# Optimization experiments

Measured on AMD Instinct MI355X. Metric: run time of the kernel, lower is better.

The kernel has to match this reference:

```python
import jax, jax.numpy as jnp
import numpy as np

D_MODEL = 1024
NUM_HEADS = 16
HEAD_DIM = D_MODEL // NUM_HEADS


def setup_inputs() -> dict:
    key = jax.random.key(0)
    kx, kq, kk, kv, ko = jax.random.split(key, 5)
    B, T = 2, 2048
    scale = 1.0 / np.sqrt(D_MODEL)
    return {
        "x": jax.random.normal(kx, (B, T, D_MODEL), dtype=jnp.float32),
        "wq": jax.random.normal(kq, (D_MODEL, D_MODEL), dtype=jnp.float32) * scale,
        "wk": jax.random.normal(kk, (D_MODEL, D_MODEL), dtype=jnp.float32) * scale,
        "wv": jax.random.normal(kv, (D_MODEL, D_MODEL), dtype=jnp.float32) * scale,
        "wo": jax.random.normal(ko, (D_MODEL, D_MODEL), dtype=jnp.float32) * scale,
    }


def _split_heads(x):
    b, t, _ = x.shape
    return x.reshape(b, t, NUM_HEADS, HEAD_DIM).transpose(0, 2, 1, 3)  # [b,h,t,d]


def reference(x, wq, wk, wv, wo):
    q = _split_heads(x @ wq)
    k = _split_heads(x @ wk)
    v = _split_heads(x @ wv)
    inv_sqrt_d = jnp.asarray(1.0 / np.sqrt(HEAD_DIM), x.dtype)
    scores = jnp.einsum("bhqd,bhkd->bhqk", q, k) * inv_sqrt_d
    weights = jax.nn.softmax(scores, axis=-1)  # dropout rate 0.0 -> identity
    out = jnp.einsum("bhqk,bhkd->bhqd", weights, v)
    b, h, t, d = out.shape
    out = out.transpose(0, 2, 1, 3).reshape(b, t, D_MODEL)
    return out @ wo
```

## Files before the change

kernel.cpp:

```cpp
#include <hip/hip_runtime.h>
#include <stdint.h>

using bf16   = __bf16;
using bf16x8 = __bf16 __attribute__((ext_vector_type(8)));
using bf16x4 = __bf16 __attribute__((ext_vector_type(4)));
using f32x4  = float  __attribute__((ext_vector_type(4)));
using f32x16 = float  __attribute__((ext_vector_type(16)));
using u32x4  = uint32_t __attribute__((ext_vector_type(4)));

#define DM 1024
#define T_ 2048
#define NH 16

__device__ __forceinline__ void gl_lds16(const void* g, void* l) {
  __builtin_amdgcn_global_load_lds(
      (__attribute__((address_space(1))) void*)g,
      (__attribute__((address_space(3))) void*)l, 16, 0, 0);
}

__device__ __forceinline__ f32x4 mfma16(bf16x8 a, bf16x8 b, f32x4 c) {
  return __builtin_amdgcn_mfma_f32_16x16x32_bf16(a, b, c, 0, 0, 0);
}
__device__ __forceinline__ f32x16 mfma32(bf16x8 a, bf16x8 b, f32x16 c) {
  return __builtin_amdgcn_mfma_f32_32x32x16_bf16(a, b, c, 0, 0, 0);
}
__device__ __forceinline__ uint32_t cvtpk(float lo, float hi) {
  uint32_t r;
  asm volatile("v_cvt_pk_bf16_f32 %0, %1, %2" : "=v"(r) : "v"(lo), "v"(hi));
  return r;
}

__global__ __launch_bounds__(256)
void k_cast_x(const float* __restrict__ x, bf16* __restrict__ xb) {
  const size_t i = (size_t)blockIdx.x * 256 + threadIdx.x;
  const float4 a = *(const float4*)(x + i * 8);
  const float4 c = *(const float4*)(x + i * 8 + 4);
  bf16x8 v;
  v[0] = (bf16)a.x; v[1] = (bf16)a.y; v[2] = (bf16)a.z; v[3] = (bf16)a.w;
  v[4] = (bf16)c.x; v[5] = (bf16)c.y; v[6] = (bf16)c.z; v[7] = (bf16)c.w;
  *(bf16x8*)(xb + i * 8) = v;
}

__global__ __launch_bounds__(256)
void k_transpose_w4(const float* __restrict__ w0, const float* __restrict__ w1,
                    const float* __restrict__ w2, const float* __restrict__ w3,
                    bf16* __restrict__ wtq, bf16* __restrict__ wto) {
  const int z = blockIdx.z;
  const float* w = (z == 0) ? w0 : (z == 1) ? w1 : (z == 2) ? w2 : w3;
  bf16* wt = (z < 3) ? (wtq + (size_t)z * 1024 * 1024) : wto;
  const float scale = (z == 0) ? 0.125f * 1.44269504f : 1.0f;
  __shared__ float tile[64][68];
  const int tx = threadIdx.x & 15;
  const int ty = threadIdx.x >> 4;
  const int k0 = blockIdx.y * 64, n0 = blockIdx.x * 64;
#pragma unroll
  for (int j = 0; j < 4; ++j) {
    const int r = ty + 16 * j;
    const float4 v = *(const float4*)(w + (size_t)(k0 + r) * DM + n0 + tx * 4);
    tile[r][tx * 4 + 0] = v.x; tile[r][tx * 4 + 1] = v.y;
    tile[r][tx * 4 + 2] = v.z; tile[r][tx * 4 + 3] = v.w;
  }
  __syncthreads();
#pragma unroll
  for (int j = 0; j < 4; ++j) {
    const int r = ty + 16 * j;
    bf16x4 o;
    o[0] = (bf16)(tile[tx * 4 + 0][r] * scale);
    o[1] = (bf16)(tile[tx * 4 + 1][r] * scale);
    o[2] = (bf16)(tile[tx * 4 + 2][r] * scale);
    o[3] = (bf16)(tile[tx * 4 + 3][r] * scale);
    *(bf16x4*)(wt + (size_t)(n0 + r) * DM + k0 + tx * 4) = o;
  }
}

template<int MODE>
__global__ __launch_bounds__(256)
void k_gemm(const bf16* __restrict__ A, const bf16* __restrict__ BT,
            bf16* __restrict__ Qg, bf16* __restrict__ Kg, bf16* __restrict__ Vt,
            float* __restrict__ Cout) {
  constexpr int BN = (MODE == 0) ? 128 : 64;
  constexpr int NTW = BN / 32;
  __shared__ __align__(16) bf16 Ash[128 * 32];
  __shared__ __align__(16) bf16 Bsh[BN * 32];
  const int tn = blockIdx.x, tm = blockIdx.y;
  const int lane = threadIdx.x & 63, w = threadIdx.x >> 6;
  const int wm = w >> 1, wn = w & 1;
  const int r16 = lane & 15, g = lane >> 4;
  f32x4 acc[4][NTW] = {};
  const bf16* Arow = A + (size_t)tm * 128 * DM;
  const bf16* Brow = BT + (size_t)tn * BN * DM;
  for (int k0 = 0; k0 < DM; k0 += 32) {
#pragma unroll
    for (int t = 0; t < 2; ++t) {
      const int q = t * 256 + w * 64 + lane;
      gl_lds16(Arow + (size_t)(q >> 2) * DM + k0 + (q & 3) * 8, Ash + (t * 256 + w * 64) * 8);
    }
#pragma unroll
    for (int t = 0; t < BN / 64; ++t) {
      const int q = t * 256 + w * 64 + lane;
      gl_lds16(Brow + (size_t)(q >> 2) * DM + k0 + (q & 3) * 8, Bsh + (t * 256 + w * 64) * 8);
    }
    __syncthreads();
    bf16x8 af[4], bfr[NTW];
#pragma unroll
    for (int mt = 0; mt < 4; ++mt)
      af[mt] = *(const bf16x8*)(Ash + (wm * 64 + mt * 16 + r16) * 32 + g * 8);
#pragma unroll
    for (int nt = 0; nt < NTW; ++nt)
      bfr[nt] = *(const bf16x8*)(Bsh + (wn * (BN / 2) + nt * 16 + r16) * 32 + g * 8);
#pragma unroll
    for (int mt = 0; mt < 4; ++mt)
#pragma unroll
      for (int nt = 0; nt < NTW; ++nt)
        acc[mt][nt] = mfma16(af[mt], bfr[nt], acc[mt][nt]);
    __syncthreads();
  }
#pragma unroll
  for (int mt = 0; mt < 4; ++mt) {
#pragma unroll
    for (int nt = 0; nt < NTW; ++nt) {
      const int ncol = tn * BN + wn * (BN / 2) + nt * 16 + r16;
      const int m0 = tm * 128 + wm * 64 + mt * 16 + g * 4;
      if (MODE == 0) {
        const int which = ncol >> 10, nl = ncol & 1023;
        const int h = nl >> 6, d = nl & 63;
        const int b = m0 >> 11, t0 = m0 & 2047;
        if (which == 2) {
          bf16x4 pv;
#pragma unroll
          for (int r = 0; r < 4; ++r) pv[r] = (bf16)acc[mt][nt][r];
          *(bf16x4*)(Vt + ((size_t)(b * NH + h) * 64 + d) * T_ + t0) = pv;
        } else {
          bf16* dst = (which == 0) ? Qg : Kg;
#pragma unroll
          for (int r = 0; r < 4; ++r)
            dst[(((size_t)(b * NH + h) * T_ + t0 + r) << 6) + d] = (bf16)acc[mt][nt][r];
        }
      } else {
#pragma unroll
        for (int r = 0; r < 4; ++r)
          Cout[(size_t)(m0 + r) * DM + ncol] = acc[mt][nt][r];
      }
    }
  }
}

__global__ __launch_bounds__(512)
void k_attn(const bf16* __restrict__ Qg, const bf16* __restrict__ Kg,
            const bf16* __restrict__ Vtr, bf16* __restrict__ Ao) {
  __shared__ __align__(16) bf16 Ksh[2][2][64 * 64];
  __shared__ __align__(16) bf16 Vsh[2][2][64 * 64];
  __shared__ float Lsh[4][64];
  const int qt = blockIdx.x, bh = blockIdx.y;
  const int lane = threadIdx.x & 63, w = threadIdx.x >> 6;
  const int qw = w & 3, kh = w >> 2;
  const int l31 = lane & 31, hi = lane >> 5;
  const bf16* Qb = Qg + (size_t)bh * T_ * 64;
  const bf16* Kb = Kg + (size_t)bh * T_ * 64;
  const bf16* Vb = Vtr + (size_t)bh * 64 * T_;
  const int q0 = qt * 128 + qw * 32;
  bf16x8 qb[4];
#pragma unroll
  for (int s = 0; s < 4; ++s)
    qb[s] = *(const bf16x8*)(Qb + (size_t)(q0 + l31) * 64 + s * 16 + hi * 8);
  f32x16 o0 = {}, o1 = {};
  float llocal = 0.f;
  const int swz31 = (l31 & 7) << 4;
  const int srow = lane >> 3;
  const int schunk = (lane & 7) ^ srow;

  auto stage = [&](int buf, int ti) {
#pragma unroll
    for (int j = 0; j < 2; ++j) {
      const int idx = qw * 2 + j;
      const int row = idx * 8 + srow;
      gl_lds16(Kb + (size_t)(ti * 64 + row) * 64 + schunk * 8, &Ksh[kh][buf][idx * 512]);
      gl_lds16(Vb + (size_t)row * T_ + ti * 64 + schunk * 8, &Vsh[kh][buf][idx * 512]);
    }
  };

  constexpr int NTH = T_ / 64 / 2;
  stage(0, kh * NTH);
  __syncthreads();
  for (int i = 0; i < NTH; ++i) {
    const int cur = i & 1;
    if (i + 1 < NTH) stage(cur ^ 1, kh * NTH + i + 1);
    const char* Kc = (const char*)Ksh[kh][cur];
    const char* Vc = (const char*)Vsh[kh][cur];
    f32x16 st0 = {}, st1 = {};
    __builtin_amdgcn_s_setprio(1);
#pragma unroll
    for (int s = 0; s < 4; ++s) {
      const int cb = (s * 32 + hi * 16) ^ swz31;
      const bf16x8 k0 = *(const bf16x8*)(Kc + l31 * 128 + cb);
      const bf16x8 k1 = *(const bf16x8*)(Kc + (32 + l31) * 128 + cb);
      st0 = mfma32(k0, qb[s], st0);
      st1 = mfma32(k1, qb[s], st1);
    }
    __builtin_amdgcn_s_setprio(0);
#pragma unroll
    for (int r = 0; r < 16; ++r) {
      st0[r] = __builtin_amdgcn_exp2f(st0[r]); llocal += st0[r];
    }
#pragma unroll
    for (int r = 0; r < 16; ++r) {
      st1[r] = __builtin_amdgcn_exp2f(st1[r]); llocal += st1[r];
    }
    __builtin_amdgcn_s_setprio(1);
#pragma unroll
    for (int s = 0; s < 4; ++s) {
      const f32x16& sv = (s < 2) ? st0 : st1;
      const int si = (s & 1) * 8;
      uint32_t a0 = cvtpk(sv[si + 0], sv[si + 1]);
      uint32_t a1 = cvtpk(sv[si + 2], sv[si + 3]);
      uint32_t b0 = cvtpk(sv[si + 4], sv[si + 5]);
      uint32_t b1 = cvtpk(sv[si + 6], sv[si + 7]);
      asm volatile("v_permlane32_swap_b32 %0, %1" : "+v"(a0), "+v"(b0));
      asm volatile("v_permlane32_swap_b32 %0, %1" : "+v"(a1), "+v"(b1));
      u32x4 fr; fr[0] = a0; fr[1] = a1; fr[2] = b0; fr[3] = b1;
      const bf16x8 pas = __builtin_bit_cast(bf16x8, fr);
      const int cb = (s * 32 + hi * 16) ^ swz31;
      const bf16x8 v0 = *(const bf16x8*)(Vc + l31 * 128 + cb);
      const bf16x8 v1 = *(const bf16x8*)(Vc + (32 + l31) * 128 + cb);
      o0 = mfma32(pas, v0, o0);
      o1 = mfma32(pas, v1, o1);
    }
    __builtin_amdgcn_s_setprio(0);
    __syncthreads();
  }
  float* cb = (float*)&Ksh[0][0][0] + qw * 2048;
  if (kh == 1) {
#pragma unroll
    for (int r = 0; r < 16; ++r) {
      cb[r * 64 + lane]        = o0[r];
      cb[(16 + r) * 64 + lane] = o1[r];
    }
    Lsh[qw][lane] = llocal;
  }
  __syncthreads();
  if (kh == 0) {
    llocal += Lsh[qw][lane];
#pragma unroll
    for (int r = 0; r < 16; ++r) {
      o0[r] += cb[r * 64 + lane];
      o1[r] += cb[(16 + r) * 64 + lane];
    }
    llocal += __shfl_xor(llocal, 32);
    const int b = bh >> 4, h = bh & 15;
#pragma unroll
    for (int r = 0; r < 16; ++r) {
      const int qoff = (r & 3) + 8 * (r >> 2) + 4 * hi;
      const float linv = 1.f / __shfl(llocal, qoff);
      const size_t base = ((size_t)(b * T_ + q0 + qoff)) * DM + h * 64 + l31;
      Ao[base]      = (bf16)(o0[r] * linv);
      Ao[base + 32] = (bf16)(o1[r] * linv);
    }
  }
}

extern "C" void kernel_launch(void* const* d_in, const int* in_sizes, int n_in,
                              void* d_out, int out_size, void* d_ws, size_t ws_size,
                              hipStream_t stream) {
  const float* x  = (const float*)d_in[0];
  const float* wq = (const float*)d_in[1];
  const float* wk = (const float*)d_in[2];
  const float* wv = (const float*)d_in[3];
  const float* wo = (const float*)d_in[4];
  char* ws = (char*)d_ws;
  const size_t MB = 1024 * 1024;
  bf16* xb   = (bf16*)(ws + 0);
  bf16* wtq  = (bf16*)(ws + 8 * MB);
  bf16* wto  = (bf16*)(ws + 14 * MB);
  bf16* Qg   = (bf16*)(ws + 16 * MB);
  bf16* Kg   = (bf16*)(ws + 24 * MB);
  bf16* Vtr  = (bf16*)(ws + 32 * MB);

  k_cast_x<<<dim3(2048), dim3(256), 0, stream>>>(x, xb);
  k_transpose_w4<<<dim3(16, 16, 4), dim3(256), 0, stream>>>(wq, wk, wv, wo, wtq, wto);
  k_gemm<0><<<dim3(24, 32), dim3(256), 0, stream>>>(xb, wtq, Qg, Kg, Vtr, (float*)nullptr);
  k_attn<<<dim3(16, 32), dim3(512), 0, stream>>>(Qg, Kg, Vtr, xb);
  k_gemm<1><<<dim3(16, 32), dim3(256), 0, stream>>>(xb, wto, (bf16*)nullptr, (bf16*)nullptr,
                                                    (bf16*)nullptr, (float*)d_out);
}
```

Baseline: 122.3 us.

## Store K and V in MFMA fragment order so attention reads them linearly

The projection GEMM epilogue now writes K and V directly in the per-lane fragment order that the attention MFMAs consume, in 64-key tiles of 4096 elements. The attention kernel stages each tile with contiguous 16-byte loads and reads fragments with lane-linear LDS accesses. This removes the XOR swizzle and its address arithmetic, and is meant to avoid LDS bank conflicts. The cost is scattered, less coalesced stores in the GEMM epilogue, especially the 2-byte strided writes for K.

Result: no change. 122.6 us (+0.2%).

```diff
diff --git a/kernel.cpp b/kernel.cpp
--- a/kernel.cpp
+++ b/kernel.cpp
@@ -76,7 +76,7 @@
 template<int MODE>
 __global__ __launch_bounds__(256)
 void k_gemm(const bf16* __restrict__ A, const bf16* __restrict__ BT,
-            bf16* __restrict__ Qg, bf16* __restrict__ Kg, bf16* __restrict__ Vt,
+            bf16* __restrict__ Qg, bf16* __restrict__ Kf, bf16* __restrict__ Vf,
             float* __restrict__ Cout) {
   constexpr int BN = (MODE == 0) ? 128 : 64;
   constexpr int NTW = BN / 32;
@@ -125,16 +125,25 @@
         const int which = ncol >> 10, nl = ncol & 1023;
         const int h = nl >> 6, d = nl & 63;
         const int b = m0 >> 11, t0 = m0 & 2047;
+        const size_t hb = (size_t)(b * NH + h) * (T_ * 64);
         if (which == 2) {
+          const int kt = t0 >> 6, s = (t0 & 63) >> 4, hi2 = (t0 >> 3) & 1, j0 = t0 & 7;
+          const int dh = d >> 5, d31 = d & 31;
           bf16x4 pv;
 #pragma unroll
           for (int r = 0; r < 4; ++r) pv[r] = (bf16)acc[mt][nt][r];
-          *(bf16x4*)(Vt + ((size_t)(b * NH + h) * 64 + d) * T_ + t0) = pv;
+          *(bf16x4*)(Vf + hb + kt * 4096 + (s * 2 + dh) * 512 + (hi2 * 32 + d31) * 8 + j0) = pv;
+        } else if (which == 1) {
+          const int kt = t0 >> 6, kh2 = (t0 >> 5) & 1;
+          const int s = d >> 4, hi2 = (d >> 3) & 1, j = d & 7;
+          bf16* base = Kf + hb + kt * 4096 + (s * 2 + kh2) * 512 + hi2 * 256 + j;
+#pragma unroll
+          for (int r = 0; r < 4; ++r)
+            base[((t0 & 31) + r) * 8] = (bf16)acc[mt][nt][r];
         } else {
-          bf16* dst = (which == 0) ? Qg : Kg;
 #pragma unroll
           for (int r = 0; r < 4; ++r)
-            dst[(((size_t)(b * NH + h) * T_ + t0 + r) << 6) + d] = (bf16)acc[mt][nt][r];
+            Qg[hb + (size_t)(t0 + r) * 64 + d] = (bf16)acc[mt][nt][r];
         }
       } else {
 #pragma unroll
@@ -146,8 +155,8 @@
 }
 
 __global__ __launch_bounds__(512)
-void k_attn(const bf16* __restrict__ Qg, const bf16* __restrict__ Kg,
-            const bf16* __restrict__ Vtr, bf16* __restrict__ Ao) {
+void k_attn(const bf16* __restrict__ Qg, const bf16* __restrict__ Kf,
+            const bf16* __restrict__ Vf, bf16* __restrict__ Ao) {
   __shared__ __align__(16) bf16 Ksh[2][2][64 * 64];
   __shared__ __align__(16) bf16 Vsh[2][2][64 * 64];
   __shared__ float Lsh[4][64];
@@ -155,9 +164,9 @@
   const int lane = threadIdx.x & 63, w = threadIdx.x >> 6;
   const int qw = w & 3, kh = w >> 2;
   const int l31 = lane & 31, hi = lane >> 5;
-  const bf16* Qb = Qg + (size_t)bh * T_ * 64;
-  const bf16* Kb = Kg + (size_t)bh * T_ * 64;
-  const bf16* Vb = Vtr + (size_t)bh * 64 * T_;
+  const bf16* Qb  = Qg + (size_t)bh * T_ * 64;
+  const bf16* Kfh = Kf + (size_t)bh * T_ * 64;
+  const bf16* Vfh = Vf + (size_t)bh * T_ * 64;
   const int q0 = qt * 128 + qw * 32;
   bf16x8 qb[4];
 #pragma unroll
@@ -165,17 +174,13 @@
     qb[s] = *(const bf16x8*)(Qb + (size_t)(q0 + l31) * 64 + s * 16 + hi * 8);
   f32x16 o0 = {}, o1 = {};
   float llocal = 0.f;
-  const int swz31 = (l31 & 7) << 4;
-  const int srow = lane >> 3;
-  const int schunk = (lane & 7) ^ srow;
 
   auto stage = [&](int buf, int ti) {
 #pragma unroll
     for (int j = 0; j < 2; ++j) {
       const int idx = qw * 2 + j;
-      const int row = idx * 8 + srow;
-      gl_lds16(Kb + (size_t)(ti * 64 + row) * 64 + schunk * 8, &Ksh[kh][buf][idx * 512]);
-      gl_lds16(Vb + (size_t)row * T_ + ti * 64 + schunk * 8, &Vsh[kh][buf][idx * 512]);
+      gl_lds16(Kfh + (size_t)ti * 4096 + idx * 512 + lane * 8, &Ksh[kh][buf][idx * 512]);
+      gl_lds16(Vfh + (size_t)ti * 4096 + idx * 512 + lane * 8, &Vsh[kh][buf][idx * 512]);
     }
   };
 
@@ -185,15 +190,14 @@
   for (int i = 0; i < NTH; ++i) {
     const int cur = i & 1;
     if (i + 1 < NTH) stage(cur ^ 1, kh * NTH + i + 1);
-    const char* Kc = (const char*)Ksh[kh][cur];
-    const char* Vc = (const char*)Vsh[kh][cur];
+    const bf16* Kc = &Ksh[kh][cur][0];
+    const bf16* Vc = &Vsh[kh][cur][0];
     f32x16 st0 = {}, st1 = {};
     __builtin_amdgcn_s_setprio(1);
 #pragma unroll
     for (int s = 0; s < 4; ++s) {
-      const int cb = (s * 32 + hi * 16) ^ swz31;
-      const bf16x8 k0 = *(const bf16x8*)(Kc + l31 * 128 + cb);
-      const bf16x8 k1 = *(const bf16x8*)(Kc + (32 + l31) * 128 + cb);
+      const bf16x8 k0 = *(const bf16x8*)(Kc + (s * 2 + 0) * 512 + lane * 8);
+      const bf16x8 k1 = *(const bf16x8*)(Kc + (s * 2 + 1) * 512 + lane * 8);
       st0 = mfma32(k0, qb[s], st0);
       st1 = mfma32(k1, qb[s], st1);
     }
@@ -219,9 +223,8 @@
       asm volatile("v_permlane32_swap_b32 %0, %1" : "+v"(a1), "+v"(b1));
       u32x4 fr; fr[0] = a0; fr[1] = a1; fr[2] = b0; fr[3] = b1;
       const bf16x8 pas = __builtin_bit_cast(bf16x8, fr);
-      const int cb = (s * 32 + hi * 16) ^ swz31;
-      const bf16x8 v0 = *(const bf16x8*)(Vc + l31 * 128 + cb);
-      const bf16x8 v1 = *(const bf16x8*)(Vc + (32 + l31) * 128 + cb);
+      const bf16x8 v0 = *(const bf16x8*)(Vc + (s * 2 + 0) * 512 + lane * 8);
+      const bf16x8 v1 = *(const bf16x8*)(Vc + (s * 2 + 1) * 512 + lane * 8);
       o0 = mfma32(pas, v0, o0);
       o1 = mfma32(pas, v1, o1);
     }
@@ -272,13 +275,13 @@
   bf16* wtq  = (bf16*)(ws + 8 * MB);
   bf16* wto  = (bf16*)(ws + 14 * MB);
   bf16* Qg   = (bf16*)(ws + 16 * MB);
-  bf16* Kg   = (bf16*)(ws + 24 * MB);
-  bf16* Vtr  = (bf16*)(ws + 32 * MB);
+  bf16* Kfb  = (bf16*)(ws + 24 * MB);
+  bf16* Vfb  = (bf16*)(ws + 32 * MB);
 
   k_cast_x<<<dim3(2048), dim3(256), 0, stream>>>(x, xb);
   k_transpose_w4<<<dim3(16, 16, 4), dim3(256), 0, stream>>>(wq, wk, wv, wo, wtq, wto);
-  k_gemm<0><<<dim3(24, 32), dim3(256), 0, stream>>>(xb, wtq, Qg, Kg, Vtr, (float*)nullptr);
-  k_attn<<<dim3(16, 32), dim3(512), 0, stream>>>(Qg, Kg, Vtr, xb);
+  k_gemm<0><<<dim3(24, 32), dim3(256), 0, stream>>>(xb, wtq, Qg, Kfb, Vfb, (float*)nullptr);
+  k_attn<<<dim3(16, 32), dim3(512), 0, stream>>>(Qg, Kfb, Vfb, xb);
   k_gemm<1><<<dim3(16, 32), dim3(256), 0, stream>>>(xb, wto, (bf16*)nullptr, (bf16*)nullptr,
                                                     (bf16*)nullptr, (float*)d_out);
 }
```
